# Performance work log

Hardware: AMD Instinct MI355X
Metric: run time of the kernel (lower is better)

The kernel has to match this reference:

```python
import jax, jax.numpy as jnp
import numpy as np

E = 1_000_000
NODE_IN = 64
EDGE_IN = 32
GLOBAL_IN = 32
HIDDEN = 128
EDGE_OUT = 32
B = 128


def setup_inputs() -> dict:
    key = jax.random.key(0)
    ks = jax.random.split(key, 10)
    src = jax.random.normal(ks[0], (E, NODE_IN), dtype=jnp.float32)
    dest = jax.random.normal(ks[1], (E, NODE_IN), dtype=jnp.float32)
    edge_attr = jax.random.normal(ks[2], (E, EDGE_IN), dtype=jnp.float32)
    u = jax.random.normal(ks[3], (B, GLOBAL_IN), dtype=jnp.float32)
    edge_batch = jnp.sort(jax.random.randint(ks[4], (E,), 0, B, dtype=jnp.int32)).astype(jnp.int64)
    in_dim = EDGE_IN + 2 * NODE_IN + GLOBAL_IN  # 192
    # Kaiming-uniform-ish init scale, values irrelevant for correctness baseline
    W1 = jax.random.normal(ks[5], (in_dim, HIDDEN), dtype=jnp.float32) * (1.0 / np.sqrt(in_dim))
    b1 = jnp.zeros((HIDDEN,), dtype=jnp.float32)
    W2 = jax.random.normal(ks[6], (HIDDEN, EDGE_OUT), dtype=jnp.float32) * (1.0 / np.sqrt(HIDDEN))
    b2 = jnp.zeros((EDGE_OUT,), dtype=jnp.float32)
    return {"src": src, "dest": dest, "edge_attr": edge_attr, "u": u,
            "edge_batch": edge_batch, "W1": W1, "b1": b1, "W2": W2, "b2": b2}


def reference(src, dest, edge_attr, u, edge_batch, W1, b1, W2, b2):
    # gather per-edge global features: [E, global_in_dim]
    u_expanded = u[edge_batch]
    # concat -> [E, edge_in + 2*node_in + global_in]
    combined = jnp.concatenate([src, dest, edge_attr, u_expanded], axis=1)
    # 2-layer MLP with ReLU
    h = jax.nn.relu(combined @ W1 + b1)
    out = h @ W2 + b2
    return out
```

## Files before the change

### kernel.cpp

```cpp
#include <hip/hip_runtime.h>

#define NODE_IN 64
#define EDGE_IN 32
#define GLOBAL_IN 32
#define HID 128
#define EOUT 32

typedef float f32x4 __attribute__((ext_vector_type(4)));
typedef float f32x2 __attribute__((ext_vector_type(2)));
typedef short s16x8 __attribute__((ext_vector_type(8)));
typedef unsigned short u16x8 __attribute__((ext_vector_type(8)));

#define XROW 384
#define HOFF 24576
#define LDSZ 40960

#define GLOADX4(dst, ptr) asm volatile("global_load_dwordx4 %0, %1, off" : "=v"(dst) : "v"(ptr))
#define GLOADD(dst, ptr)  asm volatile("global_load_dword %0, %1, off"   : "=v"(dst) : "v"(ptr))

__device__ __forceinline__ unsigned short f2bf(float f) {
  __bf16 h = (__bf16)f;
  return __builtin_bit_cast(unsigned short, h);
}

__device__ __forceinline__ s16x8 cvt8(f32x4 a, f32x4 b) {
  u16x8 v = { f2bf(a[0]), f2bf(a[1]), f2bf(a[2]), f2bf(a[3]),
              f2bf(b[0]), f2bf(b[1]), f2bf(b[2]), f2bf(b[3]) };
  return __builtin_bit_cast(s16x8, v);
}

__device__ __forceinline__ void bar_lds() {
  asm volatile("s_waitcnt lgkmcnt(0)" ::: "memory");
  __builtin_amdgcn_s_barrier();
  asm volatile("" ::: "memory");
}

__global__ __launch_bounds__(64) void prep_w(const float* __restrict__ W1,
                                             const float* __restrict__ W2,
                                             unsigned short* __restrict__ wsf) {
  const int f = blockIdx.x, l = threadIdx.x;
  const int lg = l >> 4, lr = l & 15;
  u16x8 v;
  if (f < 48) {
    const int kk = f >> 3, wd = (f >> 1) & 3, nt = f & 1;
#pragma unroll
    for (int j = 0; j < 8; ++j)
      v[j] = f2bf(W1[(32*kk + 8*lg + j)*HID + 32*wd + 2*lr + nt]);
  } else {
    const int q = f - 48, kk = q >> 1, nt = q & 1;
#pragma unroll
    for (int j = 0; j < 8; ++j)
      v[j] = f2bf(W2[(32*kk + 8*lg + j)*EOUT + 2*lr + nt]);
  }
  *(u16x8*)&wsf[f*512 + l*8] = v;
}

__global__ __launch_bounds__(256) void edge_mlp(
    const float* __restrict__ srcp, const float* __restrict__ dstp,
    const float* __restrict__ eap, const float* __restrict__ up,
    const int* __restrict__ ebp, const unsigned short* __restrict__ wsf,
    const float* __restrict__ b1, const float* __restrict__ b2,
    float* __restrict__ outp, int E, int ntiles)
{
  __shared__ __align__(16) char SM[LDSZ];

  const int t = threadIdx.x;
  const int wid = t >> 6;
  const int lane = t & 63;
  const int g = lane >> 4;
  const int r16 = lane & 15;
  const int rA = t >> 3, cA8 = (t & 7) * 8;
  const int rC = t >> 2, cC8 = (t & 3) * 8;
  const int Em1 = E - 1;

  s16x8 w1f[6][2];
#pragma unroll
  for (int kk = 0; kk < 6; ++kk) {
    w1f[kk][0] = *(const s16x8*)&wsf[(kk*8 + wid*2 + 0)*512 + lane*8];
    w1f[kk][1] = *(const s16x8*)&wsf[(kk*8 + wid*2 + 1)*512 + lane*8];
  }
  s16x8 w2f[4][2];
#pragma unroll
  for (int kk = 0; kk < 4; ++kk) {
    w2f[kk][0] = *(const s16x8*)&wsf[(48 + kk*2 + 0)*512 + lane*8];
    w2f[kk][1] = *(const s16x8*)&wsf[(48 + kk*2 + 1)*512 + lane*8];
  }
  const float b1v0 = b1[32*wid + 2*r16];
  const float b1v1 = b1[32*wid + 2*r16 + 1];
  const float b2v0 = b2[2*r16];
  const float b2v1 = b2[2*r16 + 1];

  f32x4 P0, P1, P2, P3, P4, P5, P6, P7, P8, P9, P10, P11;

  auto issue_gloads = [&](int mb, int eb) {
    const int r0 = min(mb + rA, Em1);
    const int r1 = min(mb + 32 + rA, Em1);
    const int r2 = min(mb + rC, Em1);
    const float* s0 = srcp + (size_t)r0 * NODE_IN + cA8;
    const float* s1 = srcp + (size_t)r1 * NODE_IN + cA8;
    const float* d0 = dstp + (size_t)r0 * NODE_IN + cA8;
    const float* d1 = dstp + (size_t)r1 * NODE_IN + cA8;
    const float* e0 = eap  + (size_t)r2 * EDGE_IN + cC8;
    const float* u0 = up   + (size_t)eb * GLOBAL_IN + cC8;
    GLOADX4(P0, s0);  GLOADX4(P1, s0 + 4);
    GLOADX4(P2, s1);  GLOADX4(P3, s1 + 4);
    GLOADX4(P4, d0);  GLOADX4(P5, d0 + 4);
    GLOADX4(P6, d1);  GLOADX4(P7, d1 + 4);
    GLOADX4(P8, e0);  GLOADX4(P9, e0 + 4);
    GLOADX4(P10, u0); GLOADX4(P11, u0 + 4);
  };

  const int sxw = (t & 7) ^ (rA & 7);
  const int sew = ((t & 3)     ) ^ (rC & 7);
  const int suw = (4 + (t & 3) ) ^ (rC & 7);
  auto write_x = [&]() {
    *(s16x8*)(SM + rA*XROW        + sxw*16)        = cvt8(P0, P1);
    *(s16x8*)(SM + (rA+32)*XROW   + sxw*16)        = cvt8(P2, P3);
    *(s16x8*)(SM + rA*XROW        + (8+sxw)*16)    = cvt8(P4, P5);
    *(s16x8*)(SM + (rA+32)*XROW   + (8+sxw)*16)    = cvt8(P6, P7);
    *(s16x8*)(SM + rC*XROW        + (16+sew)*16)   = cvt8(P8, P9);
    *(s16x8*)(SM + rC*XROW        + (16+suw)*16)   = cvt8(P10, P11);
  };

  int tile = blockIdx.x;
  const int TS = gridDim.x;
  int ebv;

  {
    const int eb0 = ebp[min(tile*64 + rC, Em1)];
    const int eb1 = ebp[min((tile + TS)*64 + rC, Em1)];
    issue_gloads(tile * 64, eb0);
    asm volatile("s_waitcnt vmcnt(0)" ::: "memory");
    __builtin_amdgcn_sched_barrier(0);
    write_x();
    issue_gloads((tile + TS) * 64, eb1);
    GLOADD(ebv, (ebp + min((tile + 2*TS)*64 + rC, Em1)));
  }
  bar_lds();

  for (; tile < ntiles; tile += TS) {
    const int mbase = tile * 64;

    f32x4 acc[4][2];
    {
      const f32x4 z = {0.f, 0.f, 0.f, 0.f};
#pragma unroll
      for (int mi = 0; mi < 4; ++mi) { acc[mi][0] = z; acc[mi][1] = z; }
    }
#pragma unroll
    for (int mi = 0; mi < 4; ++mi) {
      const int r = 16*mi + r16;
      const char* Rp = SM + r * XROW;
      const int s = r16 & 7;
      const s16x8 f0 = *(const s16x8*)(Rp + ((g     ^ s)      )*16);
      const s16x8 f1 = *(const s16x8*)(Rp + (((4+g) ^ s)      )*16);
      const s16x8 f2 = *(const s16x8*)(Rp + ((g     ^ s) +  8 )*16);
      const s16x8 f3 = *(const s16x8*)(Rp + (((4+g) ^ s) +  8 )*16);
      const s16x8 f4 = *(const s16x8*)(Rp + ((g     ^ s) + 16 )*16);
      const s16x8 f5 = *(const s16x8*)(Rp + (((4+g) ^ s) + 16 )*16);
      acc[mi][0] = __builtin_amdgcn_mfma_f32_16x16x32_bf16(f0, w1f[0][0], acc[mi][0], 0, 0, 0);
      acc[mi][1] = __builtin_amdgcn_mfma_f32_16x16x32_bf16(f0, w1f[0][1], acc[mi][1], 0, 0, 0);
      acc[mi][0] = __builtin_amdgcn_mfma_f32_16x16x32_bf16(f1, w1f[1][0], acc[mi][0], 0, 0, 0);
      acc[mi][1] = __builtin_amdgcn_mfma_f32_16x16x32_bf16(f1, w1f[1][1], acc[mi][1], 0, 0, 0);
      acc[mi][0] = __builtin_amdgcn_mfma_f32_16x16x32_bf16(f2, w1f[2][0], acc[mi][0], 0, 0, 0);
      acc[mi][1] = __builtin_amdgcn_mfma_f32_16x16x32_bf16(f2, w1f[2][1], acc[mi][1], 0, 0, 0);
      acc[mi][0] = __builtin_amdgcn_mfma_f32_16x16x32_bf16(f3, w1f[3][0], acc[mi][0], 0, 0, 0);
      acc[mi][1] = __builtin_amdgcn_mfma_f32_16x16x32_bf16(f3, w1f[3][1], acc[mi][1], 0, 0, 0);
      acc[mi][0] = __builtin_amdgcn_mfma_f32_16x16x32_bf16(f4, w1f[4][0], acc[mi][0], 0, 0, 0);
      acc[mi][1] = __builtin_amdgcn_mfma_f32_16x16x32_bf16(f4, w1f[4][1], acc[mi][1], 0, 0, 0);
      acc[mi][0] = __builtin_amdgcn_mfma_f32_16x16x32_bf16(f5, w1f[5][0], acc[mi][0], 0, 0, 0);
      acc[mi][1] = __builtin_amdgcn_mfma_f32_16x16x32_bf16(f5, w1f[5][1], acc[mi][1], 0, 0, 0);
    }

#pragma unroll
    for (int mi = 0; mi < 4; ++mi) {
#pragma unroll
      for (int j = 0; j < 4; ++j) {
        const float h0 = fmaxf(acc[mi][0][j] + b1v0, 0.f);
        const float h1 = fmaxf(acc[mi][1][j] + b1v1, 0.f);
        const unsigned int pk = (unsigned int)f2bf(h0) |
                                ((unsigned int)f2bf(h1) << 16);
        const int row = 16*mi + 4*g + j;
        const int ch = (4*wid + (r16 >> 2)) ^ ((4*g + j) & 7);
        *(unsigned int*)(SM + HOFF + row*256 + ch*16 + (r16 & 3)*4) = pk;
      }
    }
    bar_lds();

    asm volatile("s_waitcnt vmcnt(0)" ::: "memory");
    __builtin_amdgcn_sched_barrier(0);
    write_x();
    issue_gloads((tile + 2*TS) * 64, ebv);
    GLOADD(ebv, (ebp + min((tile + 3*TS)*64 + rC, Em1)));

    f32x4 acc2[2];
    {
      const f32x4 z = {0.f, 0.f, 0.f, 0.f};
      acc2[0] = z; acc2[1] = z;
    }
#pragma unroll
    for (int kk = 0; kk < 4; ++kk) {
      const int ch = (4*kk + g) ^ (r16 & 7);
      const s16x8 ah = *(const s16x8*)(SM + HOFF + (16*wid + r16)*256 + ch*16);
      acc2[0] = __builtin_amdgcn_mfma_f32_16x16x32_bf16(ah, w2f[kk][0], acc2[0], 0, 0, 0);
      acc2[1] = __builtin_amdgcn_mfma_f32_16x16x32_bf16(ah, w2f[kk][1], acc2[1], 0, 0, 0);
    }
#pragma unroll
    for (int j = 0; j < 4; ++j) {
      const int m = mbase + 16*wid + 4*g + j;
      if (m < E) {
        f32x2 o = { acc2[0][j] + b2v0, acc2[1][j] + b2v1 };
        *(f32x2*)(outp + (size_t)m*EOUT + 2*r16) = o;
      }
    }
    bar_lds();
  }
}

extern "C" void kernel_launch(void* const* d_in, const int* in_sizes, int n_in,
                              void* d_out, int out_size, void* d_ws, size_t ws_size,
                              hipStream_t stream) {
  const float* srcp = (const float*)d_in[0];
  const float* dstp = (const float*)d_in[1];
  const float* eap  = (const float*)d_in[2];
  const float* up   = (const float*)d_in[3];
  const int*   ebp  = (const int*)d_in[4];
  const float* W1   = (const float*)d_in[5];
  const float* b1   = (const float*)d_in[6];
  const float* W2   = (const float*)d_in[7];
  const float* b2   = (const float*)d_in[8];
  float* outp = (float*)d_out;
  unsigned short* wsf = (unsigned short*)d_ws;

  const int E = in_sizes[0] / NODE_IN;
  const int ntiles = (E + 63) / 64;
  const int grid = ntiles < 512 ? ntiles : 512;

  prep_w<<<56, 64, 0, stream>>>(W1, W2, wsf);
  edge_mlp<<<grid, 256, 0, stream>>>(srcp, dstp, eap, up, ebp, wsf, b1, b2,
                                     outp, E, ntiles);
}
```

Baseline: 162.2 us.

## Stream fp32 inputs directly to LDS with double buffering and cached u table

Replaces register-staged global loads plus bf16 conversion-on-write with async global_load_lds of raw fp32 rows into two double-buffered LDS stages, converting to bf16 at fragment-read time. The per-batch global features u are converted once into an LDS table and indexed by edge_batch instead of gathered per edge. Tiles shrink to 32 edges, the second GEMM is split across waves by output half, and vmcnt-based waits keep two stages in flight. This aims to remove the VGPR staging and serialized convert/write step, at the cost of larger LDS use, fp32 reads from LDS, and finer-grained stores.

```diff
diff --git a/kernel.cpp b/kernel.cpp
--- a/kernel.cpp
+++ b/kernel.cpp
@@ -7,16 +7,18 @@
 #define EOUT 32
 
 typedef float f32x4 __attribute__((ext_vector_type(4)));
-typedef float f32x2 __attribute__((ext_vector_type(2)));
 typedef short s16x8 __attribute__((ext_vector_type(8)));
 typedef unsigned short u16x8 __attribute__((ext_vector_type(8)));
 
-#define XROW 384
-#define HOFF 24576
-#define LDSZ 40960
-
-#define GLOADX4(dst, ptr) asm volatile("global_load_dwordx4 %0, %1, off" : "=v"(dst) : "v"(ptr))
-#define GLOADD(dst, ptr)  asm volatile("global_load_dword %0, %1, off"   : "=v"(dst) : "v"(ptr))
+#define XB0   0
+#define XB1   20480
+#define HOFF  40960
+#define UOFF  49152
+#define LDSZ  57344
+
+#define GLOADD(dst, ptr)  asm volatile("global_load_dword %0, %1, off" : "=v"(dst) : "v"(ptr))
+#define WAIT_VM7()  asm volatile("s_waitcnt vmcnt(7)"  ::: "memory")
+#define WAIT_VM11() asm volatile("s_waitcnt vmcnt(11)" ::: "memory")
 
 __device__ __forceinline__ unsigned short f2bf(float f) {
   __bf16 h = (__bf16)f;
@@ -33,6 +35,12 @@
   asm volatile("s_waitcnt lgkmcnt(0)" ::: "memory");
   __builtin_amdgcn_s_barrier();
   asm volatile("" ::: "memory");
+}
+
+__device__ __forceinline__ void glds16(const float* g, const char* l) {
+  __builtin_amdgcn_global_load_lds(
+      (const __attribute__((address_space(1))) unsigned int*)g,
+      (__attribute__((address_space(3))) unsigned int*)l, 16, 0, 0);
 }
 
 __global__ __launch_bounds__(64) void prep_w(const float* __restrict__ W1,
@@ -47,10 +55,10 @@
     for (int j = 0; j < 8; ++j)
       v[j] = f2bf(W1[(32*kk + 8*lg + j)*HID + 32*wd + 2*lr + nt]);
   } else {
-    const int q = f - 48, kk = q >> 1, nt = q & 1;
+    const int q = f - 48, kk = q >> 1, nf = q & 1;
 #pragma unroll
     for (int j = 0; j < 8; ++j)
-      v[j] = f2bf(W2[(32*kk + 8*lg + j)*EOUT + 2*lr + nt]);
+      v[j] = f2bf(W2[(32*kk + 8*lg + j)*EOUT + 16*nf + lr]);
   }
   *(u16x8*)&wsf[f*512 + l*8] = v;
 }
@@ -69,8 +77,7 @@
   const int lane = t & 63;
   const int g = lane >> 4;
   const int r16 = lane & 15;
-  const int rA = t >> 3, cA8 = (t & 7) * 8;
-  const int rC = t >> 2, cC8 = (t & 3) * 8;
+  const int mf = wid >> 1, nf = wid & 1;
   const int Em1 = E - 1;
 
   s16x8 w1f[6][2];
@@ -79,101 +86,90 @@
     w1f[kk][0] = *(const s16x8*)&wsf[(kk*8 + wid*2 + 0)*512 + lane*8];
     w1f[kk][1] = *(const s16x8*)&wsf[(kk*8 + wid*2 + 1)*512 + lane*8];
   }
-  s16x8 w2f[4][2];
-#pragma unroll
-  for (int kk = 0; kk < 4; ++kk) {
-    w2f[kk][0] = *(const s16x8*)&wsf[(48 + kk*2 + 0)*512 + lane*8];
-    w2f[kk][1] = *(const s16x8*)&wsf[(48 + kk*2 + 1)*512 + lane*8];
-  }
+  s16x8 w2f4[4];
+#pragma unroll
+  for (int kk = 0; kk < 4; ++kk)
+    w2f4[kk] = *(const s16x8*)&wsf[(48 + kk*2 + nf)*512 + lane*8];
   const float b1v0 = b1[32*wid + 2*r16];
   const float b1v1 = b1[32*wid + 2*r16 + 1];
-  const float b2v0 = b2[2*r16];
-  const float b2v1 = b2[2*r16 + 1];
-
-  f32x4 P0, P1, P2, P3, P4, P5, P6, P7, P8, P9, P10, P11;
-
-  auto issue_gloads = [&](int mb, int eb) {
-    const int r0 = min(mb + rA, Em1);
-    const int r1 = min(mb + 32 + rA, Em1);
-    const int r2 = min(mb + rC, Em1);
-    const float* s0 = srcp + (size_t)r0 * NODE_IN + cA8;
-    const float* s1 = srcp + (size_t)r1 * NODE_IN + cA8;
-    const float* d0 = dstp + (size_t)r0 * NODE_IN + cA8;
-    const float* d1 = dstp + (size_t)r1 * NODE_IN + cA8;
-    const float* e0 = eap  + (size_t)r2 * EDGE_IN + cC8;
-    const float* u0 = up   + (size_t)eb * GLOBAL_IN + cC8;
-    GLOADX4(P0, s0);  GLOADX4(P1, s0 + 4);
-    GLOADX4(P2, s1);  GLOADX4(P3, s1 + 4);
-    GLOADX4(P4, d0);  GLOADX4(P5, d0 + 4);
-    GLOADX4(P6, d1);  GLOADX4(P7, d1 + 4);
-    GLOADX4(P8, e0);  GLOADX4(P9, e0 + 4);
-    GLOADX4(P10, u0); GLOADX4(P11, u0 + 4);
-  };
-
-  const int sxw = (t & 7) ^ (rA & 7);
-  const int sew = ((t & 3)     ) ^ (rC & 7);
-  const int suw = (4 + (t & 3) ) ^ (rC & 7);
-  auto write_x = [&]() {
-    *(s16x8*)(SM + rA*XROW        + sxw*16)        = cvt8(P0, P1);
-    *(s16x8*)(SM + (rA+32)*XROW   + sxw*16)        = cvt8(P2, P3);
-    *(s16x8*)(SM + rA*XROW        + (8+sxw)*16)    = cvt8(P4, P5);
-    *(s16x8*)(SM + (rA+32)*XROW   + (8+sxw)*16)    = cvt8(P6, P7);
-    *(s16x8*)(SM + rC*XROW        + (16+sew)*16)   = cvt8(P8, P9);
-    *(s16x8*)(SM + rC*XROW        + (16+suw)*16)   = cvt8(P10, P11);
+  const float b2v  = b2[16*nf + r16];
+
+  {
+    const int row = t >> 1, half = t & 1;
+    const float* pu = up + row * GLOBAL_IN + half * 16;
+    const f32x4 u0 = *(const f32x4*)pu,       u1 = *(const f32x4*)(pu + 4);
+    const f32x4 u2 = *(const f32x4*)(pu + 8), u3 = *(const f32x4*)(pu + 12);
+    *(s16x8*)(SM + UOFF + row*64 + half*32)      = cvt8(u0, u1);
+    *(s16x8*)(SM + UOFF + row*64 + half*32 + 16) = cvt8(u2, u3);
+  }
+
+  int rowk[5]; const char* gp[5]; int pitchB[5];
+#pragma unroll
+  for (int k = 0; k < 5; ++k) {
+    const int i  = 5*wid + k;
+    const int C0 = i*64 + lane;
+    const int row = C0 / 40;
+    const int ch  = C0 - row*40;
+    const int chs = (ch & ~7) | ((ch & 7) ^ (row & 7));
+    rowk[k] = row;
+    if (ch < 16)      { gp[k] = (const char*)srcp + chs*16;      pitchB[k] = 256; }
+    else if (ch < 32) { gp[k] = (const char*)dstp + (chs-16)*16; pitchB[k] = 256; }
+    else              { gp[k] = (const char*)eap  + (chs-32)*16; pitchB[k] = 128; }
+  }
+
+  auto issue_stage = [&](int tb, int xb) {
+#pragma unroll
+    for (int k = 0; k < 5; ++k) {
+      const int gr = min(tb + rowk[k], Em1);
+      glds16((const float*)(gp[k] + (size_t)gr * pitchB[k]),
+             SM + xb + (5*wid + k)*1024);
+    }
   };
 
   int tile = blockIdx.x;
   const int TS = gridDim.x;
-  int ebv;
-
-  {
-    const int eb0 = ebp[min(tile*64 + rC, Em1)];
-    const int eb1 = ebp[min((tile + TS)*64 + rC, Em1)];
-    issue_gloads(tile * 64, eb0);
-    asm volatile("s_waitcnt vmcnt(0)" ::: "memory");
-    __builtin_amdgcn_sched_barrier(0);
-    write_x();
-    issue_gloads((tile + TS) * 64, eb1);
-    GLOADD(ebv, (ebp + min((tile + 2*TS)*64 + rC, Em1)));
-  }
+  int bbA0, bbA1, bbB0, bbB1;
+
+  issue_stage(tile*32, XB0);
+  GLOADD(bbA0, (ebp + min(tile*32 + r16,      Em1)));
+  GLOADD(bbA1, (ebp + min(tile*32 + 16 + r16, Em1)));
+  issue_stage((tile + TS)*32, XB1);
+  GLOADD(bbB0, (ebp + min((tile + TS)*32 + r16,      Em1)));
+  GLOADD(bbB1, (ebp + min((tile + TS)*32 + 16 + r16, Em1)));
+  WAIT_VM7();
+  __builtin_amdgcn_sched_barrier(0);
   bar_lds();
 
-  for (; tile < ntiles; tile += TS) {
-    const int mbase = tile * 64;
-
-    f32x4 acc[4][2];
+  auto body = [&](int tt, int xb, int& bb0, int& bb1) {
+    const int tb = tt * 32;
+
+    f32x4 acc[2][2];
     {
       const f32x4 z = {0.f, 0.f, 0.f, 0.f};
-#pragma unroll
-      for (int mi = 0; mi < 4; ++mi) { acc[mi][0] = z; acc[mi][1] = z; }
-    }
-#pragma unroll
-    for (int mi = 0; mi < 4; ++mi) {
-      const int r = 16*mi + r16;
-      const char* Rp = SM + r * XROW;
-      const int s = r16 & 7;
-      const s16x8 f0 = *(const s16x8*)(Rp + ((g     ^ s)      )*16);
-      const s16x8 f1 = *(const s16x8*)(Rp + (((4+g) ^ s)      )*16);
-      const s16x8 f2 = *(const s16x8*)(Rp + ((g     ^ s) +  8 )*16);
-      const s16x8 f3 = *(const s16x8*)(Rp + (((4+g) ^ s) +  8 )*16);
-      const s16x8 f4 = *(const s16x8*)(Rp + ((g     ^ s) + 16 )*16);
-      const s16x8 f5 = *(const s16x8*)(Rp + (((4+g) ^ s) + 16 )*16);
-      acc[mi][0] = __builtin_amdgcn_mfma_f32_16x16x32_bf16(f0, w1f[0][0], acc[mi][0], 0, 0, 0);
-      acc[mi][1] = __builtin_amdgcn_mfma_f32_16x16x32_bf16(f0, w1f[0][1], acc[mi][1], 0, 0, 0);
-      acc[mi][0] = __builtin_amdgcn_mfma_f32_16x16x32_bf16(f1, w1f[1][0], acc[mi][0], 0, 0, 0);
-      acc[mi][1] = __builtin_amdgcn_mfma_f32_16x16x32_bf16(f1, w1f[1][1], acc[mi][1], 0, 0, 0);
-      acc[mi][0] = __builtin_amdgcn_mfma_f32_16x16x32_bf16(f2, w1f[2][0], acc[mi][0], 0, 0, 0);
-      acc[mi][1] = __builtin_amdgcn_mfma_f32_16x16x32_bf16(f2, w1f[2][1], acc[mi][1], 0, 0, 0);
-      acc[mi][0] = __builtin_amdgcn_mfma_f32_16x16x32_bf16(f3, w1f[3][0], acc[mi][0], 0, 0, 0);
-      acc[mi][1] = __builtin_amdgcn_mfma_f32_16x16x32_bf16(f3, w1f[3][1], acc[mi][1], 0, 0, 0);
-      acc[mi][0] = __builtin_amdgcn_mfma_f32_16x16x32_bf16(f4, w1f[4][0], acc[mi][0], 0, 0, 0);
-      acc[mi][1] = __builtin_amdgcn_mfma_f32_16x16x32_bf16(f4, w1f[4][1], acc[mi][1], 0, 0, 0);
-      acc[mi][0] = __builtin_amdgcn_mfma_f32_16x16x32_bf16(f5, w1f[5][0], acc[mi][0], 0, 0, 0);
-      acc[mi][1] = __builtin_amdgcn_mfma_f32_16x16x32_bf16(f5, w1f[5][1], acc[mi][1], 0, 0, 0);
-    }
-
-#pragma unroll
-    for (int mi = 0; mi < 4; ++mi) {
+      acc[0][0] = z; acc[0][1] = z; acc[1][0] = z; acc[1][1] = z;
+    }
+#pragma unroll
+    for (int mi = 0; mi < 2; ++mi) {
+      const char* Xr = SM + xb + (16*mi + r16)*640;
+      const int sw = r16 & 7;
+      s16x8 fr[6];
+#pragma unroll
+      for (int kk = 0; kk < 5; ++kk) {
+        const f32x4 a = *(const f32x4*)(Xr + (8*kk + (((2*g)  ) ^ sw))*16);
+        const f32x4 b = *(const f32x4*)(Xr + (8*kk + (((2*g)|1) ^ sw))*16);
+        fr[kk] = cvt8(a, b);
+      }
+      const int bbv = mi ? bb1 : bb0;
+      fr[5] = *(const s16x8*)(SM + UOFF + bbv*64 + g*16);
+#pragma unroll
+      for (int kk = 0; kk < 6; ++kk) {
+        acc[mi][0] = __builtin_amdgcn_mfma_f32_16x16x32_bf16(fr[kk], w1f[kk][0], acc[mi][0], 0, 0, 0);
+        acc[mi][1] = __builtin_amdgcn_mfma_f32_16x16x32_bf16(fr[kk], w1f[kk][1], acc[mi][1], 0, 0, 0);
+      }
+    }
+
+#pragma unroll
+    for (int mi = 0; mi < 2; ++mi) {
 #pragma unroll
       for (int j = 0; j < 4; ++j) {
         const float h0 = fmaxf(acc[mi][0][j] + b1v0, 0.f);
@@ -187,33 +183,33 @@
     }
     bar_lds();
 
-    asm volatile("s_waitcnt vmcnt(0)" ::: "memory");
-    __builtin_amdgcn_sched_barrier(0);
-    write_x();
-    issue_gloads((tile + 2*TS) * 64, ebv);
-    GLOADD(ebv, (ebp + min((tile + 3*TS)*64 + rC, Em1)));
-
-    f32x4 acc2[2];
-    {
-      const f32x4 z = {0.f, 0.f, 0.f, 0.f};
-      acc2[0] = z; acc2[1] = z;
-    }
+    issue_stage((tt + 2*TS)*32, xb);
+    GLOADD(bb0, (ebp + min((tt + 2*TS)*32 + r16,      Em1)));
+    GLOADD(bb1, (ebp + min((tt + 2*TS)*32 + 16 + r16, Em1)));
+
+    f32x4 acc2;
+    { const f32x4 z = {0.f, 0.f, 0.f, 0.f}; acc2 = z; }
 #pragma unroll
     for (int kk = 0; kk < 4; ++kk) {
       const int ch = (4*kk + g) ^ (r16 & 7);
-      const s16x8 ah = *(const s16x8*)(SM + HOFF + (16*wid + r16)*256 + ch*16);
-      acc2[0] = __builtin_amdgcn_mfma_f32_16x16x32_bf16(ah, w2f[kk][0], acc2[0], 0, 0, 0);
-      acc2[1] = __builtin_amdgcn_mfma_f32_16x16x32_bf16(ah, w2f[kk][1], acc2[1], 0, 0, 0);
+      const s16x8 ah = *(const s16x8*)(SM + HOFF + (16*mf + r16)*256 + ch*16);
+      acc2 = __builtin_amdgcn_mfma_f32_16x16x32_bf16(ah, w2f4[kk], acc2, 0, 0, 0);
     }
 #pragma unroll
     for (int j = 0; j < 4; ++j) {
-      const int m = mbase + 16*wid + 4*g + j;
-      if (m < E) {
-        f32x2 o = { acc2[0][j] + b2v0, acc2[1][j] + b2v1 };
-        *(f32x2*)(outp + (size_t)m*EOUT + 2*r16) = o;
-      }
-    }
+      const int m = tb + 16*mf + 4*g + j;
+      if (m < E) outp[(size_t)m*EOUT + 16*nf + r16] = acc2[j] + b2v;
+    }
+
+    WAIT_VM11();
+    __builtin_amdgcn_sched_barrier(0);
     bar_lds();
+  };
+
+  for (; tile < ntiles; tile += 2*TS) {
+    body(tile, XB0, bbA0, bbA1);
+    if (tile + TS < ntiles)
+      body(tile + TS, XB1, bbB0, bbB1);
   }
 }
 
@@ -233,7 +229,7 @@
   unsigned short* wsf = (unsigned short*)d_ws;
 
   const int E = in_sizes[0] / NODE_IN;
-  const int ntiles = (E + 63) / 64;
+  const int ntiles = (E + 31) / 32;
   const int grid = ntiles < 512 ? ntiles : 512;
 
   prep_w<<<56, 64, 0, stream>>>(W1, W2, wsf);
```

Result: slower. 165.6 us (+2.1%).
